# Kernel tuning notes

Hardware: AMD Instinct MI355X
Metric: run time of the kernel (lower is better)

## Reference

```python
import jax, jax.numpy as jnp
import numpy as np

B, N, C_IN = 8, 16384, 64
NPOINTS = 1024     # S: number of sampled centers (FPS)
NNEI = 32          # K: neighbors per center (ball query cap)
RADIUS = 0.2
EPS = 1e-5


def fps(pos, S):
    """Farthest point sampling, deterministic start at index 0. pos: [B,N,3] -> [B,S] int32."""
    b, n, _ = pos.shape

    def step(carry, _):
        dist, far = carry
        centroid = jnp.take_along_axis(pos, far[:, None, None], axis=1)  # [B,1,3]
        d = jnp.sum((pos - centroid) ** 2, axis=-1)                       # [B,N]
        dist = jnp.minimum(dist, d)
        return (dist, jnp.argmax(dist, axis=-1).astype(jnp.int32)), far

    init = (jnp.full((b, n), 1e10, pos.dtype), jnp.zeros((b,), jnp.int32))
    _, cent = jax.lax.scan(step, init, None, length=S)  # [S,B]
    return cent.T                                        # [B,S]


def gather(points, idx):
    """points [B,N,C], idx [B,...] -> [B,...,C] (per-batch fancy gather)."""
    return jax.vmap(lambda p, i: p[i])(points, idx)


def ball_query(pos, centers, radius, k):
    """Fixed-radius neighbor search. pos [B,N,3], centers [B,S,3] -> idx [B,S,K] int32.
    Pads short neighborhoods with the first in-radius point (the center itself)."""
    n = pos.shape[1]
    sqr = jnp.sum((centers[:, :, None, :] - pos[:, None, :, :]) ** 2, axis=-1)  # [B,S,N]
    idx = jnp.where(sqr <= radius * radius, jnp.arange(n, dtype=jnp.int32), n)
    idx = jnp.sort(idx, axis=-1)[..., :k]                                        # [B,S,K]
    first = idx[..., :1]
    return jnp.where(idx == n, first, idx)


def conv_bn_relu(x, w, b, g, be):
    """1x1 Conv2d + BatchNorm2d(training stats) + ReLU over grouped tensor x [B,S,K,Cin]."""
    h = jnp.einsum('bskc,cd->bskd', x, w) + b
    mu = jnp.mean(h, axis=(0, 1, 2), keepdims=True)
    var = jnp.mean((h - mu) ** 2, axis=(0, 1, 2), keepdims=True)
    h = (h - mu) * jax.lax.rsqrt(var + EPS) * g + be
    return jax.nn.relu(h)


def reference(pos, feat,
              w_sem1, b_sem1, g_sem1, be_sem1, w_sem2, b_sem2, g_sem2, be_sem2,
              w_geo1, b_geo1, g_geo1, be_geo1, w_geo2, b_geo2, g_geo2, be_geo2):
    centroids = fps(pos, NPOINTS)                       # [B,S]
    centers = gather(pos, centroids)                    # [B,S,3]
    idx = ball_query(pos, centers, RADIUS, NNEI)        # [B,S,K]

    grouped_pos = gather(pos, idx)                      # [B,S,K,3]
    grouped_feat = gather(feat, idx)                    # [B,S,K,C]
    center_rep = jnp.broadcast_to(centers[:, :, None, :], grouped_pos.shape)
    geo_in = jnp.concatenate([center_rep, grouped_pos], axis=-1)  # [B,S,K,6]

    h = conv_bn_relu(grouped_feat, w_sem1, b_sem1, g_sem1, be_sem1)
    h = conv_bn_relu(h, w_sem2, b_sem2, g_sem2, be_sem2)
    h_sem = jnp.max(h, axis=2)                          # [B,S,Cout] max-pool over neighbors

    hg = conv_bn_relu(geo_in, w_geo1, b_geo1, g_geo1, be_geo1)
    hg = conv_bn_relu(hg, w_geo2, b_geo2, g_geo2, be_geo2)
    h_geo = jnp.max(hg, axis=2)                         # [B,S,Cout]

    # original concatenates semantic and geo node features along dim 0
    return jnp.concatenate([h_sem, h_geo], axis=0)      # [2B,S,Cout]


def setup_inputs() -> dict:
    key = jax.random.key(0)
    ks = jax.random.split(key, 12)
    d = {
        'pos': jax.random.uniform(ks[0], (B, N, 3), jnp.float32),
        'feat': jax.random.normal(ks[1], (B, N, C_IN), jnp.float32),
        'w_sem1': jax.random.normal(ks[2], (64, 64), jnp.float32) * 0.05,
        'b_sem1': jnp.zeros((64,), jnp.float32),
        'g_sem1': jnp.ones((64,), jnp.float32),
        'be_sem1': jnp.zeros((64,), jnp.float32),
        'w_sem2': jax.random.normal(ks[3], (64, 128), jnp.float32) * 0.05,
        'b_sem2': jnp.zeros((128,), jnp.float32),
        'g_sem2': jnp.ones((128,), jnp.float32),
        'be_sem2': jnp.zeros((128,), jnp.float32),
        'w_geo1': jax.random.normal(ks[4], (6, 64), jnp.float32) * 0.05,
        'b_geo1': jnp.zeros((64,), jnp.float32),
        'g_geo1': jnp.ones((64,), jnp.float32),
        'be_geo1': jnp.zeros((64,), jnp.float32),
        'w_geo2': jax.random.normal(ks[5], (64, 128), jnp.float32) * 0.05,
        'b_geo2': jnp.zeros((128,), jnp.float32),
        'g_geo2': jnp.ones((128,), jnp.float32),
        'be_geo2': jnp.zeros((128,), jnp.float32),
    }
    return d
```

## Files before the change

kernel.cpp:

```cpp
#include <hip/hip_runtime.h>

#define NB 8
#define NPTS 16384
#define S 1024
#define KNEI 32
#define MROWS (NB*S*KNEI)

typedef float v2f __attribute__((ext_vector_type(2)));

#define DPP_MAXF0(CTRL, v) do {                                               \
    int _o = __builtin_amdgcn_update_dpp(0, __float_as_int(v),                \
                                         (CTRL), 0xF, 0xF, true);             \
    (v) = fmaxf((v), __int_as_float(_o));                                     \
  } while (0)

#define DPP_MINI(CTRL, v) do {                                                \
    int _o = __builtin_amdgcn_update_dpp((int)0x7fffffff, (v),                \
                                         (CTRL), 0xF, 0xF, false);            \
    (v) = (_o < (v)) ? _o : (v);                                              \
  } while (0)

#define DPP_MAXK0(CTRL, k) do {                                               \
    int _olo = __builtin_amdgcn_update_dpp(0, (int)(unsigned)(k),             \
                                           (CTRL), 0xF, 0xF, true);           \
    int _ohi = __builtin_amdgcn_update_dpp(0, (int)(unsigned)((k) >> 32),     \
                                           (CTRL), 0xF, 0xF, true);           \
    unsigned long long _ok = (((unsigned long long)(unsigned)_ohi) << 32)     \
                           | (unsigned)_olo;                                  \
    if (_ok > (k)) (k) = _ok;                                                 \
  } while (0)

#define DPP_ROW_SHR1   0x111
#define DPP_ROW_SHR2   0x112
#define DPP_ROW_SHR4   0x114
#define DPP_ROW_SHR8   0x118
#define DPP_ROW_BCAST15 0x142
#define DPP_ROW_BCAST31 0x143

__global__ __launch_bounds__(1024, 4) void fps_kernel(const float* __restrict__ pos,
                                                      float* __restrict__ centers,
                                                      float* __restrict__ sbuf){
#pragma clang fp contract(off)
  __shared__ int hist[4096];
  __shared__ int ts[1024];
  __shared__ unsigned short perm[16384];
  __shared__ unsigned long long lslot[2][16];
  const int b = blockIdx.x;
  const int t = threadIdx.x;
  const int wid = t >> 6, lane = t & 63;
  const float* pb = pos + (size_t)b * NPTS * 3;
  float* ssx = sbuf + (size_t)b * 3 * NPTS;
  float* ssy = ssx + NPTS;
  float* ssz = ssy + NPTS;
  const int p0 = t * 16;

  float c[48];
  {
    const float4* src = (const float4*)(pb + (size_t)t*48);
#pragma unroll
    for (int q = 0; q < 12; ++q) *(float4*)&c[q*4] = src[q];
  }
  int cell[16];
#pragma unroll
  for (int j = 0; j < 16; ++j){
    float x = c[3*j], y = c[3*j+1], z = c[3*j+2];
    int ix = (int)(x * 16.f); ix = ix < 0 ? 0 : (ix > 15 ? 15 : ix);
    int iy = (int)(y * 16.f); iy = iy < 0 ? 0 : (iy > 15 ? 15 : iy);
    int iz = (int)(z * 16.f); iz = iz < 0 ? 0 : (iz > 15 ? 15 : iz);
    int m = 0;
#pragma unroll
    for (int k = 0; k < 4; ++k){
      m |= ((ix >> k) & 1) << (3*k + 2);
      m |= ((iy >> k) & 1) << (3*k + 1);
      m |= ((iz >> k) & 1) << (3*k + 0);
    }
    cell[j] = m;
  }
#pragma unroll
  for (int i = 0; i < 4; ++i) hist[t*4 + i] = 0;
  __syncthreads();
#pragma unroll
  for (int j = 0; j < 16; ++j) atomicAdd(&hist[cell[j]], 1);
  __syncthreads();
  int h0 = hist[t*4], h1 = hist[t*4+1], h2v = hist[t*4+2], h3 = hist[t*4+3];
  (void)h3;
  ts[t] = h0 + h1 + h2v + hist[t*4+3];
  __syncthreads();
  for (int off = 1; off < 1024; off <<= 1){
    int add = (t >= off) ? ts[t - off] : 0;
    __syncthreads();
    ts[t] += add;
    __syncthreads();
  }
  {
    int base = (t == 0) ? 0 : ts[t-1];
    hist[t*4]   = base;
    hist[t*4+1] = base + h0;
    hist[t*4+2] = base + h0 + h1;
    hist[t*4+3] = base + h0 + h1 + h2v;
  }
  __syncthreads();
#pragma unroll
  for (int j = 0; j < 16; ++j){
    int dst = atomicAdd(&hist[cell[j]], 1);
    ssx[dst] = c[3*j];
    ssy[dst] = c[3*j+1];
    ssz[dst] = c[3*j+2];
    perm[dst] = (unsigned short)(p0 + j);
  }
  __syncthreads();

  v2f px[8], py[8], pz[8], dist[8];
#pragma unroll
  for (int g = 0; g < 4; ++g){
    float4 vx = *(const float4*)&ssx[p0 + g*4];
    float4 vy = *(const float4*)&ssy[p0 + g*4];
    float4 vz = *(const float4*)&ssz[p0 + g*4];
    px[g*2]   = (v2f){vx.x, vx.y}; px[g*2+1] = (v2f){vx.z, vx.w};
    py[g*2]   = (v2f){vy.x, vy.y}; py[g*2+1] = (v2f){vy.z, vy.w};
    pz[g*2]   = (v2f){vz.x, vz.y}; pz[g*2+1] = (v2f){vz.z, vz.w};
  }
  float bxl = 1e30f, bxh = -1e30f, byl = 1e30f, byh = -1e30f;
  float bzl = 1e30f, bzh = -1e30f;
#pragma unroll
  for (int j = 0; j < 8; ++j){
    asm volatile("" : "+v"(px[j]), "+v"(py[j]), "+v"(pz[j]));
    bxl = fminf(bxl, fminf(px[j].x, px[j].y));
    bxh = fmaxf(bxh, fmaxf(px[j].x, px[j].y));
    byl = fminf(byl, fminf(py[j].x, py[j].y));
    byh = fmaxf(byh, fmaxf(py[j].x, py[j].y));
    bzl = fminf(bzl, fminf(pz[j].x, pz[j].y));
    bzh = fmaxf(bzh, fmaxf(pz[j].x, pz[j].y));
    dist[j] = (v2f){1e10f, 1e10f};
  }
  float ub = 1e10f;
  float cx = pb[0], cy = pb[1], cz = pb[2];

  for (int s = 0; s < S; ++s){
    if (t == 0){
      float* cd = centers + (size_t)(b*S + s)*3;
      cd[0] = cx; cd[1] = cy; cd[2] = cz;
    }
    float lx = fmaxf(fmaxf(bxl - cx, cx - bxh), 0.f);
    float ly = fmaxf(fmaxf(byl - cy, cy - byh), 0.f);
    float lz = fmaxf(fmaxf(bzl - cz, cz - bzh), 0.f);
    float lb2 = ((lx*lx + ly*ly) + lz*lz);
    if (!(lb2 * 0.99999f >= ub)){
      v2f cx2 = (v2f){cx, cx}, cy2 = (v2f){cy, cy}, cz2 = (v2f){cz, cz};
      float nb = 0.0f;
#pragma unroll
      for (int j = 0; j < 8; ++j){
        v2f dx = px[j] - cx2;
        v2f dy = py[j] - cy2;
        v2f dz = pz[j] - cz2;
        v2f t1 = dx * dx;
        v2f t2 = dy * dy;
        v2f t3 = dz * dz;
        v2f d  = (t1 + t2) + t3;
        v2f od = dist[j];
        v2f nd = (v2f){__builtin_fminf(od.x, d.x), __builtin_fminf(od.y, d.y)};
        dist[j] = nd;
        nb = fmaxf(fmaxf(nb, nd.x), nd.y);
      }
      ub = nb;
    }
    float bv = ub;
    DPP_MAXF0(DPP_ROW_SHR1,   bv);
    DPP_MAXF0(DPP_ROW_SHR2,   bv);
    DPP_MAXF0(DPP_ROW_SHR4,   bv);
    DPP_MAXF0(DPP_ROW_SHR8,   bv);
    DPP_MAXF0(DPP_ROW_BCAST15, bv);
    DPP_MAXF0(DPP_ROW_BCAST31, bv);
    float bmw = __int_as_float(
        __builtin_amdgcn_readlane(__float_as_int(bv), 63));
    int mi = 0x7fffffff;
    if (ub == bmw){
#pragma unroll
      for (int j = 0; j < 8; ++j){
        if (dist[j].x == bmw){ int o = (int)perm[p0 + 2*j];     mi = o < mi ? o : mi; }
        if (dist[j].y == bmw){ int o = (int)perm[p0 + 2*j + 1]; mi = o < mi ? o : mi; }
      }
    }
    DPP_MINI(DPP_ROW_SHR1,   mi);
    DPP_MINI(DPP_ROW_SHR2,   mi);
    DPP_MINI(DPP_ROW_SHR4,   mi);
    DPP_MINI(DPP_ROW_SHR8,   mi);
    DPP_MINI(DPP_ROW_BCAST15, mi);
    DPP_MINI(DPP_ROW_BCAST31, mi);
    int miw = __builtin_amdgcn_readlane(mi, 63);
    const int par = s & 1;
    if (lane == 0){
      lslot[par][wid] = ((unsigned long long)__float_as_uint(bmw) << 15)
                      | (unsigned long long)(16384 - miw);
    }
    __syncthreads();
    unsigned long long kk = lslot[par][lane & 15];
    DPP_MAXK0(DPP_ROW_SHR1, kk);
    DPP_MAXK0(DPP_ROW_SHR2, kk);
    DPP_MAXK0(DPP_ROW_SHR4, kk);
    DPP_MAXK0(DPP_ROW_SHR8, kk);
    unsigned klo = (unsigned)__builtin_amdgcn_readlane((int)(unsigned)kk, 15);
    unsigned khi = (unsigned)__builtin_amdgcn_readlane((int)(unsigned)(kk >> 32), 15);
    unsigned long long kmax = (((unsigned long long)khi) << 32) | klo;
    int ufi = 16384 - (int)(kmax & 0x7FFFull);
    const float* cp = pb + (size_t)ufi*3;
    cx = cp[0]; cy = cp[1]; cz = cp[2];
  }
}

__global__ __launch_bounds__(256) void ballq_kernel(const float* __restrict__ pos,
                                                    const float* __restrict__ centers,
                                                    int* __restrict__ idx){
#pragma clang fp contract(off)
  const float R2 = (float)(0.2*0.2);
  int wid  = blockIdx.x*4 + (threadIdx.x >> 6);
  int lane = threadIdx.x & 63;
  int b = wid >> 10;
  const float* pb = pos + (size_t)b * NPTS * 3;
  float cx = centers[wid*3+0], cy = centers[wid*3+1], cz = centers[wid*3+2];
  int* out = idx + wid*KNEI;
  int count = 0; int first = -1;
  for (int base = 0; base < NPTS; base += 64){
    int p = base + lane;
    float dx = pb[p*3+0]-cx, dy = pb[p*3+1]-cy, dz = pb[p*3+2]-cz;
    float t1 = dx*dx, t2 = dy*dy, t3 = dz*dz;
    float d = (t1 + t2) + t3;
    bool inr = d <= R2;
    unsigned long long mask = __ballot(inr);
    if (count == 0 && mask) first = base + __builtin_ctzll(mask);
    if (inr){
      int slot = count + __popcll(mask & ((1ull << lane) - 1ull));
      if (slot < KNEI) out[slot] = p;
    }
    count += __popcll(mask);
    if (count >= KNEI) break;
  }
  if (count < KNEI){
    for (int slot = count + lane; slot < KNEI; slot += 64) out[slot] = first;
  }
}

__global__ __launch_bounds__(256) void gemm_sem1(const float* __restrict__ feat,
    const int* __restrict__ idx, const float* __restrict__ w,
    const float* __restrict__ bias, float* __restrict__ h1,
    float* __restrict__ stat){
  __shared__ float xs[64][68];
  __shared__ float wsh[64][64];
  const int tid = threadIdx.x;
  const int m0 = blockIdx.x * 64;
#pragma unroll
  for (int i = 0; i < 4; ++i){
    int q = tid + i*256;
    int r = q >> 4, c4 = q & 15;
    *(float4*)&wsh[r][c4*4] = *(const float4*)&w[r*64 + c4*4];
  }
#pragma unroll
  for (int i = 0; i < 4; ++i){
    int q = tid + i*256;
    int r = q >> 4, c4 = q & 15;
    int m = m0 + r;
    int nb = idx[m];
    int b = m >> 15;
    const float* fr = feat + ((size_t)b*NPTS + nb)*64;
    *(float4*)&xs[r][c4*4] = *(const float4*)&fr[c4*4];
  }
  __syncthreads();
  const int g  = tid & 7;
  const int rt = tid >> 3;
  const int r0 = rt * 2;
  float acc[2][8];
#pragma unroll
  for (int c = 0; c < 8; ++c){ float bb = bias[g*8+c]; acc[0][c] = bb; acc[1][c] = bb; }
  for (int k = 0; k < 64; ++k){
    float x0 = xs[r0][k], x1 = xs[r0+1][k];
    float4 wa = *(float4*)&wsh[k][g*8];
    float4 wb = *(float4*)&wsh[k][g*8+4];
    float wv[8] = {wa.x,wa.y,wa.z,wa.w,wb.x,wb.y,wb.z,wb.w};
#pragma unroll
    for (int c = 0; c < 8; ++c){ acc[0][c] += x0*wv[c]; acc[1][c] += x1*wv[c]; }
  }
#pragma unroll
  for (int r = 0; r < 2; ++r){
    float* dst = h1 + (size_t)(m0 + r0 + r)*64 + g*8;
    *(float4*)dst     = make_float4(acc[r][0],acc[r][1],acc[r][2],acc[r][3]);
    *(float4*)(dst+4) = make_float4(acc[r][4],acc[r][5],acc[r][6],acc[r][7]);
  }
  float ls[8], lq[8];
#pragma unroll
  for (int c = 0; c < 8; ++c){
    ls[c] = acc[0][c] + acc[1][c];
    lq[c] = acc[0][c]*acc[0][c] + acc[1][c]*acc[1][c];
  }
  __syncthreads();
  float* red  = &xs[0][0];
  float* redq = &wsh[0][0];
#pragma unroll
  for (int c = 0; c < 8; ++c){
    red[(g*8+c)*32 + rt]  = ls[c];
    redq[(g*8+c)*32 + rt] = lq[c];
  }
  __syncthreads();
  if (tid < 128){
    int c = tid & 63;
    const float* src = (tid < 64) ? red : redq;
    float a2 = 0.f;
    for (int i = 0; i < 32; ++i) a2 += src[c*32+i];
    atomicAdd(&stat[(tid < 64 ? 0 : 64) + c], a2);
  }
}

__global__ __launch_bounds__(256) void gemm2_kernel(const float* __restrict__ hin,
    const float* __restrict__ abn, const float* __restrict__ dbn,
    const float* __restrict__ w, const float* __restrict__ bias,
    float* __restrict__ hout, float* __restrict__ stat){
  __shared__ float xs[64][68];
  __shared__ float wsh[64][128];
  const int tid = threadIdx.x;
  const int m0 = blockIdx.x * 64;
#pragma unroll
  for (int i = 0; i < 8; ++i){
    int q = tid + i*256;
    int r = q >> 5, c4 = q & 31;
    *(float4*)&wsh[r][c4*4] = *(const float4*)&w[r*128 + c4*4];
  }
#pragma unroll
  for (int i = 0; i < 4; ++i){
    int q = tid + i*256;
    int r = q >> 4, c4 = q & 15;
    float4 v  = *(const float4*)&hin[(size_t)(m0+r)*64 + c4*4];
    float4 av = *(const float4*)&abn[c4*4];
    float4 dv = *(const float4*)&dbn[c4*4];
    v.x = fmaxf(v.x*av.x + dv.x, 0.f);
    v.y = fmaxf(v.y*av.y + dv.y, 0.f);
    v.z = fmaxf(v.z*av.z + dv.z, 0.f);
    v.w = fmaxf(v.w*av.w + dv.w, 0.f);
    *(float4*)&xs[r][c4*4] = v;
  }
  __syncthreads();
  const int g  = tid & 15;
  const int rt = tid >> 4;
  const int r0 = rt * 4;
  float acc[4][8];
#pragma unroll
  for (int c = 0; c < 8; ++c){
    float bb = bias[g*8+c];
    acc[0][c]=bb; acc[1][c]=bb; acc[2][c]=bb; acc[3][c]=bb;
  }
  for (int k = 0; k < 64; ++k){
    float x0 = xs[r0][k], x1 = xs[r0+1][k], x2 = xs[r0+2][k], x3 = xs[r0+3][k];
    float4 wa = *(float4*)&wsh[k][g*8];
    float4 wb = *(float4*)&wsh[k][g*8+4];
    float wv[8] = {wa.x,wa.y,wa.z,wa.w,wb.x,wb.y,wb.z,wb.w};
#pragma unroll
    for (int c = 0; c < 8; ++c){
      acc[0][c] += x0*wv[c]; acc[1][c] += x1*wv[c];
      acc[2][c] += x2*wv[c]; acc[3][c] += x3*wv[c];
    }
  }
#pragma unroll
  for (int r = 0; r < 4; ++r){
    float* dst = hout + (size_t)(m0 + r0 + r)*128 + g*8;
    *(float4*)dst     = make_float4(acc[r][0],acc[r][1],acc[r][2],acc[r][3]);
    *(float4*)(dst+4) = make_float4(acc[r][4],acc[r][5],acc[r][6],acc[r][7]);
  }
  float ls[8], lq[8];
#pragma unroll
  for (int c = 0; c < 8; ++c){
    ls[c] = acc[0][c]+acc[1][c]+acc[2][c]+acc[3][c];
    lq[c] = acc[0][c]*acc[0][c]+acc[1][c]*acc[1][c]+acc[2][c]*acc[2][c]+acc[3][c]*acc[3][c];
  }
  __syncthreads();
  float* red = &xs[0][0];
#pragma unroll
  for (int c = 0; c < 8; ++c){
    red[(g*8+c)*16 + rt]        = ls[c];
    red[2048 + (g*8+c)*16 + rt] = lq[c];
  }
  __syncthreads();
  {
    int c = tid & 127;
    int isq = tid >> 7;
    float a2 = 0.f;
    for (int i = 0; i < 16; ++i) a2 += red[isq*2048 + c*16 + i];
    atomicAdd(&stat[isq*128 + c], a2);
  }
}

__global__ __launch_bounds__(256) void gemm_geo1(const float* __restrict__ pos,
    const float* __restrict__ centers, const int* __restrict__ idx,
    const float* __restrict__ w, const float* __restrict__ bias,
    float* __restrict__ hout, float* __restrict__ stat){
  __shared__ float xs[64][8];
  __shared__ float wsh[6][64];
  __shared__ float red[2048];
  __shared__ float redq[2048];
  const int tid = threadIdx.x;
  const int m0 = blockIdx.x * 64;
  for (int i = tid; i < 384; i += 256) wsh[i >> 6][i & 63] = w[i];
  if (tid < 64){
    int m = m0 + tid;
    int grp = m >> 5;
    int b = m >> 15;
    int nb = idx[m];
    const float* cp = centers + (size_t)grp*3;
    const float* pp = pos + ((size_t)b*NPTS + nb)*3;
    xs[tid][0]=cp[0]; xs[tid][1]=cp[1]; xs[tid][2]=cp[2];
    xs[tid][3]=pp[0]; xs[tid][4]=pp[1]; xs[tid][5]=pp[2];
  }
  __syncthreads();
  const int g  = tid & 7;
  const int rt = tid >> 3;
  const int r0 = rt * 2;
  float acc[2][8];
#pragma unroll
  for (int c = 0; c < 8; ++c){ float bb = bias[g*8+c]; acc[0][c]=bb; acc[1][c]=bb; }
#pragma unroll
  for (int k = 0; k < 6; ++k){
    float x0 = xs[r0][k], x1 = xs[r0+1][k];
    float4 wa = *(float4*)&wsh[k][g*8];
    float4 wb = *(float4*)&wsh[k][g*8+4];
    float wv[8] = {wa.x,wa.y,wa.z,wa.w,wb.x,wb.y,wb.z,wb.w};
#pragma unroll
    for (int c = 0; c < 8; ++c){ acc[0][c] += x0*wv[c]; acc[1][c] += x1*wv[c]; }
  }
#pragma unroll
  for (int r = 0; r < 2; ++r){
    float* dst = hout + (size_t)(m0 + r0 + r)*64 + g*8;
    *(float4*)dst     = make_float4(acc[r][0],acc[r][1],acc[r][2],acc[r][3]);
    *(float4*)(dst+4) = make_float4(acc[r][4],acc[r][5],acc[r][6],acc[r][7]);
  }
  float ls[8], lq[8];
#pragma unroll
  for (int c = 0; c < 8; ++c){
    ls[c] = acc[0][c] + acc[1][c];
    lq[c] = acc[0][c]*acc[0][c] + acc[1][c]*acc[1][c];
  }
#pragma unroll
  for (int c = 0; c < 8; ++c){
    red[(g*8+c)*32 + rt]  = ls[c];
    redq[(g*8+c)*32 + rt] = lq[c];
  }
  __syncthreads();
  if (tid < 128){
    int c = tid & 63;
    const float* src = (tid < 64) ? red : redq;
    float a2 = 0.f;
    for (int i = 0; i < 32; ++i) a2 += src[c*32+i];
    atomicAdd(&stat[(tid < 64 ? 0 : 64) + c], a2);
  }
}

__global__ void bn_finalize(const float* __restrict__ stat,
                            const float* __restrict__ gam, const float* __restrict__ bet,
                            float* __restrict__ a, float* __restrict__ d, int C){
  int c = threadIdx.x;
  if (c >= C) return;
  const float invM = 1.0f / (float)MROWS;
  float mu  = stat[c] * invM;
  float ex2 = stat[C + c] * invM;
  float var = ex2 - mu*mu;
  float aa = gam[c] * rsqrtf(var + 1e-5f);
  a[c] = aa;
  d[c] = bet[c] - mu*aa;
}

__global__ __launch_bounds__(256) void maxpool_kernel(const float* __restrict__ hin,
    const float* __restrict__ abn, const float* __restrict__ dbn,
    float* __restrict__ out){
  const int tid = threadIdx.x;
  const int grp = blockIdx.x*8 + (tid >> 5);
  const int c4 = tid & 31;
  const float* base = hin + (size_t)grp*KNEI*128 + c4*4;
  float4 a = *(const float4*)&abn[c4*4];
  float4 d = *(const float4*)&dbn[c4*4];
  float4 m = make_float4(-3.4e38f,-3.4e38f,-3.4e38f,-3.4e38f);
  for (int k = 0; k < KNEI; ++k){
    float4 v = *(const float4*)&base[(size_t)k*128];
    m.x = fmaxf(m.x, v.x*a.x + d.x);
    m.y = fmaxf(m.y, v.y*a.y + d.y);
    m.z = fmaxf(m.z, v.z*a.z + d.z);
    m.w = fmaxf(m.w, v.w*a.w + d.w);
  }
  m.x = fmaxf(m.x, 0.f); m.y = fmaxf(m.y, 0.f);
  m.z = fmaxf(m.z, 0.f); m.w = fmaxf(m.w, 0.f);
  *(float4*)&out[(size_t)grp*128 + c4*4] = m;
}

__global__ void zero_kernel(float* __restrict__ p, int n){
  int i = blockIdx.x*blockDim.x + threadIdx.x;
  if (i < n) p[i] = 0.f;
}

extern "C" void kernel_launch(void* const* d_in, const int* in_sizes, int n_in,
                              void* d_out, int out_size, void* d_ws, size_t ws_size,
                              hipStream_t stream){
  const float* pos   = (const float*)d_in[0];
  const float* feat  = (const float*)d_in[1];
  const float* w_s1  = (const float*)d_in[2];
  const float* b_s1  = (const float*)d_in[3];
  const float* g_s1  = (const float*)d_in[4];
  const float* be_s1 = (const float*)d_in[5];
  const float* w_s2  = (const float*)d_in[6];
  const float* b_s2  = (const float*)d_in[7];
  const float* g_s2  = (const float*)d_in[8];
  const float* be_s2 = (const float*)d_in[9];
  const float* w_g1  = (const float*)d_in[10];
  const float* b_g1  = (const float*)d_in[11];
  const float* g_g1  = (const float*)d_in[12];
  const float* be_g1 = (const float*)d_in[13];
  const float* w_g2  = (const float*)d_in[14];
  const float* b_g2  = (const float*)d_in[15];
  const float* g_g2  = (const float*)d_in[16];
  const float* be_g2 = (const float*)d_in[17];
  float* outp = (float*)d_out;
  float* wsf  = (float*)d_ws;

  float* centers = wsf;
  int*   idxp    = (int*)(wsf + 24576);
  float* stats   = wsf + 24576 + 262144;
  float* bnad    = stats + 768;
  float* h1      = wsf + 288256;
  float* h2      = h1 + (size_t)MROWS*64;
  float* sortbuf = h2;

  float* st1 = stats;
  float* st2 = stats + 128;
  float* st3 = stats + 384;
  float* st4 = stats + 512;
  float* a1 = bnad;        float* d1 = bnad + 64;
  float* a2 = bnad + 128;  float* d2 = bnad + 256;
  float* a3 = bnad + 384;  float* d3 = bnad + 448;
  float* a4 = bnad + 512;  float* d4 = bnad + 640;

  zero_kernel<<<3, 256, 0, stream>>>(stats, 768);
  fps_kernel<<<NB, 1024, 0, stream>>>(pos, centers, sortbuf);
  ballq_kernel<<<(NB*S)/4, 256, 0, stream>>>(pos, centers, idxp);

  gemm_sem1<<<MROWS/64, 256, 0, stream>>>(feat, idxp, w_s1, b_s1, h1, st1);
  bn_finalize<<<1, 128, 0, stream>>>(st1, g_s1, be_s1, a1, d1, 64);
  gemm2_kernel<<<MROWS/64, 256, 0, stream>>>(h1, a1, d1, w_s2, b_s2, h2, st2);
  bn_finalize<<<1, 128, 0, stream>>>(st2, g_s2, be_s2, a2, d2, 128);
  maxpool_kernel<<<(NB*S)/8, 256, 0, stream>>>(h2, a2, d2, outp);

  gemm_geo1<<<MROWS/64, 256, 0, stream>>>(pos, centers, idxp, w_g1, b_g1, h1, st3);
  bn_finalize<<<1, 128, 0, stream>>>(st3, g_g1, be_g1, a3, d3, 64);
  gemm2_kernel<<<MROWS/64, 256, 0, stream>>>(h1, a3, d3, w_g2, b_g2, h2, st4);
  bn_finalize<<<1, 128, 0, stream>>>(st4, g_g2, be_g2, a4, d4, 128);
  maxpool_kernel<<<(NB*S)/8, 256, 0, stream>>>(h2, a4, d4, outp + (size_t)NB*S*128);
}
```

Before: 1.959 ms.

## Restructure FPS argmax with per-lane keys and shared-memory winner coordinates

The FPS loop now computes a packed (distance, index) key per lane only when that lane's points were updated, and reduces it with a single 64-bit DPP max instead of separate float-max and int-min passes. The winning lane publishes the next centroid's coordinates to shared memory, so the global-memory reload of the chosen point is removed from the serial loop. Permutation indices are kept in registers instead of being read from LDS each iteration. In exchange, the 64-bit DPP reduction costs more instructions per step and register pressure goes up.

```diff
diff --git a/kernel.cpp b/kernel.cpp
--- a/kernel.cpp
+++ b/kernel.cpp
@@ -7,18 +7,6 @@
 #define MROWS (NB*S*KNEI)
 
 typedef float v2f __attribute__((ext_vector_type(2)));
-
-#define DPP_MAXF0(CTRL, v) do {                                               \
-    int _o = __builtin_amdgcn_update_dpp(0, __float_as_int(v),                \
-                                         (CTRL), 0xF, 0xF, true);             \
-    (v) = fmaxf((v), __int_as_float(_o));                                     \
-  } while (0)
-
-#define DPP_MINI(CTRL, v) do {                                                \
-    int _o = __builtin_amdgcn_update_dpp((int)0x7fffffff, (v),                \
-                                         (CTRL), 0xF, 0xF, false);            \
-    (v) = (_o < (v)) ? _o : (v);                                              \
-  } while (0)
 
 #define DPP_MAXK0(CTRL, k) do {                                               \
     int _olo = __builtin_amdgcn_update_dpp(0, (int)(unsigned)(k),             \
@@ -44,7 +32,8 @@
   __shared__ int hist[4096];
   __shared__ int ts[1024];
   __shared__ unsigned short perm[16384];
-  __shared__ unsigned long long lslot[2][16];
+  __shared__ unsigned long long lslotK[2][16];
+  __shared__ float lslotX[2][16], lslotY[2][16], lslotZ[2][16];
   const int b = blockIdx.x;
   const int t = threadIdx.x;
   const int wid = t >> 6, lane = t & 63;
@@ -82,8 +71,7 @@
 #pragma unroll
   for (int j = 0; j < 16; ++j) atomicAdd(&hist[cell[j]], 1);
   __syncthreads();
-  int h0 = hist[t*4], h1 = hist[t*4+1], h2v = hist[t*4+2], h3 = hist[t*4+3];
-  (void)h3;
+  int h0 = hist[t*4], h1 = hist[t*4+1], h2v = hist[t*4+2];
   ts[t] = h0 + h1 + h2v + hist[t*4+3];
   __syncthreads();
   for (int off = 1; off < 1024; off <<= 1){
@@ -111,6 +99,7 @@
   __syncthreads();
 
   v2f px[8], py[8], pz[8], dist[8];
+  int perm_reg[8];
 #pragma unroll
   for (int g = 0; g < 4; ++g){
     float4 vx = *(const float4*)&ssx[p0 + g*4];
@@ -120,11 +109,15 @@
     py[g*2]   = (v2f){vy.x, vy.y}; py[g*2+1] = (v2f){vy.z, vy.w};
     pz[g*2]   = (v2f){vz.x, vz.y}; pz[g*2+1] = (v2f){vz.z, vz.w};
   }
+#pragma unroll
+  for (int j = 0; j < 8; ++j){
+    perm_reg[j] = (int)perm[p0 + 2*j] | ((int)perm[p0 + 2*j + 1] << 16);
+  }
   float bxl = 1e30f, bxh = -1e30f, byl = 1e30f, byh = -1e30f;
   float bzl = 1e30f, bzh = -1e30f;
 #pragma unroll
   for (int j = 0; j < 8; ++j){
-    asm volatile("" : "+v"(px[j]), "+v"(py[j]), "+v"(pz[j]));
+    asm volatile("" : "+v"(px[j]), "+v"(py[j]), "+v"(pz[j]), "+v"(perm_reg[j]));
     bxl = fminf(bxl, fminf(px[j].x, px[j].y));
     bxh = fmaxf(bxh, fmaxf(px[j].x, px[j].y));
     byl = fminf(byl, fminf(py[j].x, py[j].y));
@@ -134,6 +127,9 @@
     dist[j] = (v2f){1e10f, 1e10f};
   }
   float ub = 1e10f;
+  int mi = 0;
+  unsigned long long key = 0;
+  int iswin = 0;
   float cx = pb[0], cy = pb[1], cz = pb[2];
 
   for (int s = 0; s < S; ++s){
@@ -145,66 +141,78 @@
     float ly = fmaxf(fmaxf(byl - cy, cy - byh), 0.f);
     float lz = fmaxf(fmaxf(bzl - cz, cz - bzh), 0.f);
     float lb2 = ((lx*lx + ly*ly) + lz*lz);
-    if (!(lb2 * 0.99999f >= ub)){
-      v2f cx2 = (v2f){cx, cx}, cy2 = (v2f){cy, cy}, cz2 = (v2f){cz, cz};
-      float nb = 0.0f;
+    bool act = !(lb2 * 0.99999f >= ub);
+    unsigned long long am = __ballot((int)act);
+    if (am){
+      if (act){
+        v2f cx2 = (v2f){cx, cx}, cy2 = (v2f){cy, cy}, cz2 = (v2f){cz, cz};
+        float nb = 0.0f;
+#pragma unroll
+        for (int j = 0; j < 8; ++j){
+          v2f dx = px[j] - cx2;
+          v2f dy = py[j] - cy2;
+          v2f dz = pz[j] - cz2;
+          v2f t1 = dx * dx;
+          v2f t2 = dy * dy;
+          v2f t3 = dz * dz;
+          v2f d  = (t1 + t2) + t3;
+          v2f od = dist[j];
+          v2f nd = (v2f){__builtin_fminf(od.x, d.x), __builtin_fminf(od.y, d.y)};
+          dist[j] = nd;
+          nb = fmaxf(fmaxf(nb, nd.x), nd.y);
+        }
+        ub = nb;
+        int m2 = 0x7fffffff;
+#pragma unroll
+        for (int j = 0; j < 8; ++j){
+          if (dist[j].x == ub){ int o = perm_reg[j] & 0xffff;          m2 = o < m2 ? o : m2; }
+          if (dist[j].y == ub){ int o = (perm_reg[j] >> 16) & 0xffff;  m2 = o < m2 ? o : m2; }
+        }
+        mi = m2;
+        key = ((unsigned long long)__float_as_uint(ub) << 15)
+            | (unsigned long long)(16384 - mi);
+      }
+      unsigned long long wk = key;
+      DPP_MAXK0(DPP_ROW_SHR1,   wk);
+      DPP_MAXK0(DPP_ROW_SHR2,   wk);
+      DPP_MAXK0(DPP_ROW_SHR4,   wk);
+      DPP_MAXK0(DPP_ROW_SHR8,   wk);
+      DPP_MAXK0(DPP_ROW_BCAST15, wk);
+      DPP_MAXK0(DPP_ROW_BCAST31, wk);
+      unsigned klo = (unsigned)__builtin_amdgcn_readlane((int)(unsigned)wk, 63);
+      unsigned khi = (unsigned)__builtin_amdgcn_readlane((int)(unsigned)(wk >> 32), 63);
+      unsigned long long kmax = (((unsigned long long)khi) << 32) | klo;
+      unsigned long long wmask = __ballot((int)(key == kmax));
+      iswin = (lane == (int)__builtin_ctzll(wmask));
+    }
+    const int par = s & 1;
+    if (iswin){
+      float wx = cx, wy = cy, wz = cz;
 #pragma unroll
       for (int j = 0; j < 8; ++j){
-        v2f dx = px[j] - cx2;
-        v2f dy = py[j] - cy2;
-        v2f dz = pz[j] - cz2;
-        v2f t1 = dx * dx;
-        v2f t2 = dy * dy;
-        v2f t3 = dz * dz;
-        v2f d  = (t1 + t2) + t3;
-        v2f od = dist[j];
-        v2f nd = (v2f){__builtin_fminf(od.x, d.x), __builtin_fminf(od.y, d.y)};
-        dist[j] = nd;
-        nb = fmaxf(fmaxf(nb, nd.x), nd.y);
+        if ((perm_reg[j] & 0xffff) == mi)        { wx = px[j].x; wy = py[j].x; wz = pz[j].x; }
+        if (((perm_reg[j] >> 16) & 0xffff) == mi){ wx = px[j].y; wy = py[j].y; wz = pz[j].y; }
       }
-      ub = nb;
-    }
-    float bv = ub;
-    DPP_MAXF0(DPP_ROW_SHR1,   bv);
-    DPP_MAXF0(DPP_ROW_SHR2,   bv);
-    DPP_MAXF0(DPP_ROW_SHR4,   bv);
-    DPP_MAXF0(DPP_ROW_SHR8,   bv);
-    DPP_MAXF0(DPP_ROW_BCAST15, bv);
-    DPP_MAXF0(DPP_ROW_BCAST31, bv);
-    float bmw = __int_as_float(
-        __builtin_amdgcn_readlane(__float_as_int(bv), 63));
-    int mi = 0x7fffffff;
-    if (ub == bmw){
-#pragma unroll
-      for (int j = 0; j < 8; ++j){
-        if (dist[j].x == bmw){ int o = (int)perm[p0 + 2*j];     mi = o < mi ? o : mi; }
-        if (dist[j].y == bmw){ int o = (int)perm[p0 + 2*j + 1]; mi = o < mi ? o : mi; }
-      }
-    }
-    DPP_MINI(DPP_ROW_SHR1,   mi);
-    DPP_MINI(DPP_ROW_SHR2,   mi);
-    DPP_MINI(DPP_ROW_SHR4,   mi);
-    DPP_MINI(DPP_ROW_SHR8,   mi);
-    DPP_MINI(DPP_ROW_BCAST15, mi);
-    DPP_MINI(DPP_ROW_BCAST31, mi);
-    int miw = __builtin_amdgcn_readlane(mi, 63);
-    const int par = s & 1;
-    if (lane == 0){
-      lslot[par][wid] = ((unsigned long long)__float_as_uint(bmw) << 15)
-                      | (unsigned long long)(16384 - miw);
+      lslotK[par][wid] = key;
+      lslotX[par][wid] = wx;
+      lslotY[par][wid] = wy;
+      lslotZ[par][wid] = wz;
     }
     __syncthreads();
-    unsigned long long kk = lslot[par][lane & 15];
+    unsigned long long kk = lslotK[par][lane & 15];
+    unsigned long long kko = kk;
     DPP_MAXK0(DPP_ROW_SHR1, kk);
     DPP_MAXK0(DPP_ROW_SHR2, kk);
     DPP_MAXK0(DPP_ROW_SHR4, kk);
     DPP_MAXK0(DPP_ROW_SHR8, kk);
-    unsigned klo = (unsigned)__builtin_amdgcn_readlane((int)(unsigned)kk, 15);
-    unsigned khi = (unsigned)__builtin_amdgcn_readlane((int)(unsigned)(kk >> 32), 15);
-    unsigned long long kmax = (((unsigned long long)khi) << 32) | klo;
-    int ufi = 16384 - (int)(kmax & 0x7FFFull);
-    const float* cp = pb + (size_t)ufi*3;
-    cx = cp[0]; cy = cp[1]; cz = cp[2];
+    unsigned blo = (unsigned)__builtin_amdgcn_readlane((int)(unsigned)kk, 15);
+    unsigned bhi = (unsigned)__builtin_amdgcn_readlane((int)(unsigned)(kk >> 32), 15);
+    unsigned long long bkmax = (((unsigned long long)bhi) << 32) | blo;
+    unsigned m16 = (unsigned)__ballot((int)(kko == bkmax)) & 0xffffu;
+    int sidx = (int)__builtin_ctz(m16);
+    cx = lslotX[par][sidx];
+    cy = lslotY[par][sidx];
+    cz = lslotZ[par][sidx];
   }
 }
 
```

Measured after the change: 2.330 ms. 1.19x slower.
